# Kernel tuning notes

Hardware: AMD Instinct MI355X
Metric: run time of the kernel (lower is better)

## Reference

```python
import jax, jax.numpy as jnp
import numpy as np

N_USERS = 100_000
N_ITEMS = 200_000
N_EDGES = 1_000_000
D = 64        # in_size == every layer_size
L = 3         # number of NGCF layers
B = 4096      # BPR batch
SLOPE = 0.2   # LeakyReLU negative slope
EPS = 1e-12   # F.normalize eps


def setup_inputs() -> dict:
    key = jax.random.key(0)
    ks = jax.random.split(key, 11)
    s = 1.0 / np.sqrt(D)  # xavier-ish scale
    return dict(
        user_feat=jax.random.normal(ks[0], (N_USERS, D), jnp.float32) * s,
        item_feat=jax.random.normal(ks[1], (N_ITEMS, D), jnp.float32) * s,
        W1=jax.random.normal(ks[2], (L, D, D), jnp.float32) * s,
        b1=jnp.zeros((L, D), jnp.float32),
        W2=jax.random.normal(ks[3], (L, D, D), jnp.float32) * s,
        b2=jnp.zeros((L, D), jnp.float32),
        edge_src=jax.random.randint(ks[4], (N_EDGES,), 0, N_USERS),
        edge_dst=jax.random.randint(ks[5], (N_EDGES,), 0, N_ITEMS),
        users=jax.random.randint(ks[6], (B,), 0, N_USERS),
        pos_items=jax.random.randint(ks[7], (B,), 0, N_ITEMS),
        neg_items=jax.random.randint(ks[8], (B,), 0, N_ITEMS),
    )


def _act_norm(h):
    # LeakyReLU(0.2) -> (dropout=identity, eval) -> row-wise L2 normalize
    h = jax.nn.leaky_relu(h, SLOPE)
    n = jnp.linalg.norm(h, axis=1, keepdims=True)
    return h / jnp.maximum(n, EPS)


def _ngcf_forward(user_feat, item_feat, W1, b1, W2, b2, edge_src, edge_dst):
    ones = jnp.ones((edge_src.shape[0],), user_feat.dtype)
    deg_u = jax.ops.segment_sum(ones, edge_src, num_segments=N_USERS)  # out-degree of users
    deg_i = jax.ops.segment_sum(ones, edge_dst, num_segments=N_ITEMS)  # in-degree of items
    norm = (deg_u[edge_src] * deg_i[edge_dst]) ** -0.5  # [E], same for both directions
    norm = norm[:, None]

    hu, hi = user_feat, item_feat
    u_embeds, i_embeds = [hu], [hi]
    for l in range(L):
        # per-edge elementwise product term (shared between both directions)
        p = hu[edge_src] * hi[edge_dst]            # [E, D]
        pw = p @ W2[l] + b2[l]                     # [E, D]
        # user -> item messages, summed per item
        m_i = norm * ((hu @ W1[l] + b1[l])[edge_src] + pw)
        # item -> user messages, summed per user
        m_u = norm * ((hi @ W1[l] + b1[l])[edge_dst] + pw)
        hi_new = jax.ops.segment_sum(m_i, edge_dst, num_segments=N_ITEMS)
        hu_new = jax.ops.segment_sum(m_u, edge_src, num_segments=N_USERS)
        hu, hi = _act_norm(hu_new), _act_norm(hi_new)
        u_embeds.append(hu)
        i_embeds.append(hi)

    user_embd = jnp.concatenate(u_embeds, axis=1)  # [N_USERS, D*(L+1)]
    item_embd = jnp.concatenate(i_embeds, axis=1)  # [N_ITEMS, D*(L+1)]
    return user_embd, item_embd


def reference(user_feat, item_feat, W1, b1, W2, b2,
              edge_src, edge_dst, users, pos_items, neg_items):
    user_embd, item_embd = _ngcf_forward(
        user_feat, item_feat, W1, b1, W2, b2, edge_src, edge_dst)
    return (user_embd[users], item_embd[pos_items], item_embd[neg_items])
```

## Files before the change

### kernel.cpp

```cpp
#include <hip/hip_runtime.h>

#define NU 100000
#define NI 200000
#define NE 1000000
#define NB 4096
#define CAP 16384
#define NBS 98
#define NBD 98
#define NTI (NI / 16)
#define NTU (NU / 16)
#define DBKT 64
#define CAPD 65536
#define NBI 196
#define NBU 98

typedef __attribute__((ext_vector_type(8))) short bf16x8;
typedef __attribute__((ext_vector_type(4))) float f32x4;
typedef __attribute__((ext_vector_type(8))) unsigned short u16x8;

static __device__ __forceinline__ short f2bf(float f) {
  unsigned u = __builtin_bit_cast(unsigned, f);
  unsigned r = (u + 0x7fffu + ((u >> 16) & 1u)) >> 16;
  return (short)r;
}
static __device__ __forceinline__ float bf2f(unsigned short u) {
  return __builtin_bit_cast(float, ((unsigned)u) << 16);
}

__global__ __launch_bounds__(256) void binA_kernel(const int* __restrict__ src,
                                                   const int* __restrict__ dst,
                                                   int* __restrict__ gcur_s,
                                                   int* __restrict__ gcur_d,
                                                   int2* __restrict__ temp_s,
                                                   int2* __restrict__ temp_d) {
  __shared__ int lh[128], lbase[128], lpos[128];
  const int dir = blockIdx.x >> 9;
  const int cb = blockIdx.x & 511;
  const int lo = (int)(((long long)NE * cb) >> 9);
  const int hi = (int)(((long long)NE * (cb + 1)) >> 9);
  const int* key = dir ? dst : src;
  const int* oth = dir ? src : dst;
  int* gcur = dir ? gcur_d : gcur_s;
  int2* temp = dir ? temp_d : temp_s;
  const int shift = dir ? 11 : 10;
  const int tid = threadIdx.x;
  if (tid < 128) lh[tid] = 0;
  __syncthreads();
  for (int e = lo + tid; e < hi; e += 256) atomicAdd(&lh[key[e] >> shift], 1);
  __syncthreads();
  if (tid < 128) {
    const int c = lh[tid];
    lbase[tid] = c ? atomicAdd(&gcur[tid], c) : 0;
    lpos[tid] = 0;
  }
  __syncthreads();
  for (int e = lo + tid; e < hi; e += 256) {
    const int k = key[e];
    const int b = k >> shift;
    const int p = lbase[b] + atomicAdd(&lpos[b], 1);
    temp[(size_t)b * CAP + p] = make_int2(k, oth[e]);
  }
}

__global__ void bktscan_kernel(const int* __restrict__ gcur_s, const int* __restrict__ gcur_d,
                               int* __restrict__ bktofs_s, int* __restrict__ bktofs_d,
                               int* __restrict__ ofs_u, int* __restrict__ ofs_i) {
  const int t = threadIdx.x;
  if (t == 0) {
    int a = 0;
    for (int i = 0; i < NBS; ++i) { bktofs_s[i] = a; a += gcur_s[i]; }
    bktofs_s[NBS] = a;
    ofs_u[NU] = NE;
  }
  if (t == 1) {
    int a = 0;
    for (int i = 0; i < NBD; ++i) { bktofs_d[i] = a; a += gcur_d[i]; }
    bktofs_d[NBD] = a;
    ofs_i[NI] = NE;
  }
}

__global__ __launch_bounds__(256) void placeB_kernel(const int2* __restrict__ temp_s,
                                                     const int2* __restrict__ temp_d,
                                                     const int* __restrict__ gcur_s,
                                                     const int* __restrict__ gcur_d,
                                                     const int* __restrict__ bktofs_s,
                                                     const int* __restrict__ bktofs_d,
                                                     int* __restrict__ ofs_u, int* __restrict__ ofs_i,
                                                     int* __restrict__ by_src, int* __restrict__ by_dst) {
  __shared__ int cnt[2048];
  __shared__ int exc[2048];
  __shared__ int wsum[256];
  const bool isdst = blockIdx.x >= NBS;
  const int b = isdst ? (int)blockIdx.x - NBS : (int)blockIdx.x;
  const int shift = isdst ? 11 : 10;
  const int nodelo = b << shift;
  const int n = isdst ? NI : NU;
  const int2* temp = (isdst ? temp_d : temp_s) + (size_t)b * CAP;
  const int ecnt = (isdst ? gcur_d : gcur_s)[b];
  const int bbase = (isdst ? bktofs_d : bktofs_s)[b];
  int* ofs = isdst ? ofs_i : ofs_u;
  int* by = isdst ? by_dst : by_src;
  const int tid = threadIdx.x;
  const int NN = 1 << shift;

  for (int j = tid; j < NN; j += 256) cnt[j] = 0;
  __syncthreads();
  for (int k = tid; k < ecnt; k += 256) atomicAdd(&cnt[temp[k].x - nodelo], 1);
  __syncthreads();
  const int per = NN >> 8;
  int s = 0;
  for (int j = 0; j < per; ++j) s += cnt[tid * per + j];
  wsum[tid] = s;
  __syncthreads();
  for (int off = 1; off < 256; off <<= 1) {
    int t2 = (tid >= off) ? wsum[tid - off] : 0;
    __syncthreads();
    wsum[tid] += t2;
    __syncthreads();
  }
  int run = wsum[tid] - s;
  for (int j = 0; j < per; ++j) {
    const int idx = tid * per + j;
    exc[idx] = run;
    run += cnt[idx];
  }
  __syncthreads();
  for (int j = tid; j < NN; j += 256) {
    const int node = nodelo + j;
    if (node < n) ofs[node] = bbase + exc[j];
  }
  __syncthreads();
  for (int j = tid; j < NN; j += 256) cnt[j] = exc[j];
  __syncthreads();
  for (int k = tid; k < ecnt; k += 256) {
    const int2 t2 = temp[k];
    const int p = bbase + atomicAdd(&cnt[t2.x - nodelo], 1);
    by[p] = t2.y;
  }
}

__global__ __launch_bounds__(256) void dbinA_kernel(const int* __restrict__ ofs_i,
                                                    const int* __restrict__ ofs_u,
                                                    int* __restrict__ dgcur,
                                                    int* __restrict__ arena_i,
                                                    int* __restrict__ arena_u) {
  __shared__ int lh[DBKT], lbase[DBKT], lpos[DBKT];
  const bool item = blockIdx.x < NBI;
  const int b = item ? (int)blockIdx.x : (int)blockIdx.x - NBI;
  const int n = item ? NI : NU;
  const int* ofs = item ? ofs_i : ofs_u;
  int* cur = dgcur + (item ? 0 : DBKT);
  int* arena = item ? arena_i : arena_u;
  const int nodelo = b << 10;
  const int nodehi = min(nodelo + 1024, n);
  const int tid = threadIdx.x;
  if (tid < DBKT) lh[tid] = 0;
  __syncthreads();
  for (int node = nodelo + tid; node < nodehi; node += 256)
    atomicAdd(&lh[min(ofs[node + 1] - ofs[node], DBKT - 1)], 1);
  __syncthreads();
  if (tid < DBKT) {
    const int c = lh[tid];
    lbase[tid] = c ? atomicAdd(&cur[tid], c) : 0;
    lpos[tid] = 0;
  }
  __syncthreads();
  for (int node = nodelo + tid; node < nodehi; node += 256) {
    const int d = min(ofs[node + 1] - ofs[node], DBKT - 1);
    const int p = lbase[d] + atomicAdd(&lpos[d], 1);
    arena[d * CAPD + p] = node;
  }
}

__global__ void dbktscan_kernel(const int* __restrict__ dgcur,
                                int* __restrict__ dofs, int* __restrict__ dedge,
                                int* __restrict__ ofs2_i, int* __restrict__ ofs2_u) {
  const int t = threadIdx.x;
  if (t == 0) {
    int a = 0, e = 0;
    for (int d = 0; d < DBKT; ++d) { dofs[d] = a; dedge[d] = e; a += dgcur[d]; e += dgcur[d] * d; }
    dedge[DBKT] = NE;
    ofs2_i[NI] = NE;
  }
  if (t == 1) {
    int a = 0, e = 0;
    for (int d = 0; d < DBKT; ++d) {
      dofs[DBKT + d] = a; dedge[65 + d] = e;
      a += dgcur[DBKT + d]; e += dgcur[DBKT + d] * d;
    }
    dedge[65 + DBKT] = NE;
    ofs2_u[NU] = NE;
  }
}

__global__ __launch_bounds__(256) void dcompact_kernel(const int* __restrict__ dgcur,
                                                       const int* __restrict__ dofs,
                                                       const int* __restrict__ dedge,
                                                       const int* __restrict__ arena_i,
                                                       const int* __restrict__ arena_u,
                                                       int* __restrict__ perm_i, int* __restrict__ perm_u,
                                                       int* __restrict__ inv_i, int* __restrict__ inv_u,
                                                       int* __restrict__ ofs2_i, int* __restrict__ ofs2_u,
                                                       float* __restrict__ rs2_i, float* __restrict__ rs2_u) {
  const int bk = blockIdx.x;
  const bool item = bk < DBKT;
  const int d = item ? bk : bk - DBKT;
  const int cnt = dgcur[bk];
  const int nodebase = dofs[bk];
  const int edgebase = dedge[item ? d : 65 + d];
  const int* arena = item ? arena_i : arena_u;
  int* perm = item ? perm_i : perm_u;
  int* inv = item ? inv_i : inv_u;
  int* ofs2 = item ? ofs2_i : ofs2_u;
  float* rs2 = item ? rs2_i : rs2_u;
  const float rsv = d ? rsqrtf((float)d) : 0.f;
  for (int k = threadIdx.x; k < cnt; k += 256) {
    const int node = arena[d * CAPD + k];
    const int r = nodebase + k;
    perm[r] = node;
    inv[node] = r;
    ofs2[r] = edgebase + k * d;
    rs2[r] = rsv;
  }
}

__global__ __launch_bounds__(256) void remap3_kernel(const int* __restrict__ ofs_i,
                                                     const int* __restrict__ ofs_u,
                                                     const int* __restrict__ ofs2_i,
                                                     const int* __restrict__ ofs2_u,
                                                     const int* __restrict__ perm_i,
                                                     const int* __restrict__ perm_u,
                                                     const int* __restrict__ inv_i,
                                                     const int* __restrict__ inv_u,
                                                     const int* __restrict__ by_dst,
                                                     const int* __restrict__ by_src,
                                                     const float* __restrict__ rs2_u,
                                                     const float* __restrict__ rs2_i,
                                                     int* __restrict__ by2_dst,
                                                     int* __restrict__ by2_src,
                                                     float* __restrict__ c_i,
                                                     float* __restrict__ c_u) {
  int r = blockIdx.x * 256 + threadIdx.x;
  const int *ofs, *ofs2, *perm, *invo, *by;
  const float *rso, *rsw;
  int* by2;
  float* c;
  int rr;
  if (r < NI) {
    rr = r; ofs = ofs_i; ofs2 = ofs2_i; perm = perm_i; invo = inv_u;
    by = by_dst; rso = rs2_u; rsw = rs2_i; by2 = by2_dst; c = c_i;
  } else if (r < NI + NU) {
    rr = r - NI; ofs = ofs_u; ofs2 = ofs2_u; perm = perm_u; invo = inv_i;
    by = by_src; rso = rs2_i; rsw = rs2_u; by2 = by2_src; c = c_u;
  } else return;
  const int lo2 = ofs2[rr];
  const int d = ofs2[rr + 1] - lo2;
  float sum = 0.f;
  if (d > 0) {
    const int oo = ofs[perm[rr]];
    for (int k0 = 0; k0 < d; k0 += 4) {
      int v4[4], nv[4];
#pragma unroll
      for (int s = 0; s < 4; ++s) v4[s] = by[oo + min(k0 + s, d - 1)];
#pragma unroll
      for (int s = 0; s < 4; ++s) nv[s] = invo[v4[s]];
#pragma unroll
      for (int s = 0; s < 4; ++s)
        if (k0 + s < d) {
          by2[lo2 + k0 + s] = nv[s];
          sum += rso[nv[s]];
        }
    }
  }
  c[rr] = rsw[rr] * sum;
}

__global__ __launch_bounds__(256) void obuild_kernel(const int* __restrict__ users,
                                                     const int* __restrict__ pos,
                                                     const int* __restrict__ neg,
                                                     const int* __restrict__ inv_u,
                                                     const int* __restrict__ inv_i,
                                                     int* __restrict__ head_u,
                                                     int* __restrict__ head_i,
                                                     int* __restrict__ nxt) {
  const int s = blockIdx.x * 256 + threadIdx.x;
  if (s >= 3 * NB) return;
  const int which = s / NB, b = s - which * NB;
  const int row = (which == 0) ? users[b] : ((which == 1) ? pos[b] : neg[b]);
  int node;
  int* head;
  if (which == 0) { node = inv_u[row]; head = head_u; }
  else            { node = inv_i[row]; head = head_i; }
  nxt[s] = atomicExch(&head[node], s);
}

__global__ __launch_bounds__(256) void conv_kernel(const float* __restrict__ uf,
                                                   const float* __restrict__ itf,
                                                   const int* __restrict__ perm_u,
                                                   const int* __restrict__ perm_i,
                                                   const float* __restrict__ rs2_u,
                                                   const float* __restrict__ rs2_i,
                                                   unsigned short* __restrict__ hsu,
                                                   unsigned short* __restrict__ hsi) {
  int i = blockIdx.x * 256 + threadIdx.x;
  const int n4u = NU * 16;
  const float* in;
  const int* perm;
  const float* rs;
  unsigned short* outp;
  int j;
  if (i < n4u) {
    in = uf; perm = perm_u; rs = rs2_u; outp = hsu; j = i;
  } else if (i < n4u + NI * 16) {
    in = itf; perm = perm_i; rs = rs2_i; outp = hsi; j = i - n4u;
  } else return;
  const int rnew = j >> 4;
  const int grp = j & 15;
  const float rsn = rs[rnew];
  float4 v = *(const float4*)&in[(size_t)perm[rnew] * 64 + grp * 4];
  ushort4 o;
  o.x = (unsigned short)f2bf(v.x * rsn);
  o.y = (unsigned short)f2bf(v.y * rsn);
  o.z = (unsigned short)f2bf(v.z * rsn);
  o.w = (unsigned short)f2bf(v.w * rsn);
  *(ushort4*)&outp[(size_t)j * 4] = o;
}

__global__ __launch_bounds__(256) void layer_fused_kernel(const int* __restrict__ ofs2_i,
                                                          const int* __restrict__ ofs2_u,
                                                          const int* __restrict__ by2_dst,
                                                          const int* __restrict__ by2_src,
                                                          const float* __restrict__ rs2_u,
                                                          const float* __restrict__ rs2_i,
                                                          const float* __restrict__ c_i,
                                                          const float* __restrict__ c_u,
                                                          const unsigned short* __restrict__ hsu,
                                                          const unsigned short* __restrict__ hsi,
                                                          const float* __restrict__ W1,
                                                          const float* __restrict__ b1,
                                                          const float* __restrict__ W2,
                                                          const float* __restrict__ b2,
                                                          const int* __restrict__ head_i,
                                                          const int* __restrict__ head_u,
                                                          const int* __restrict__ nxt,
                                                          float* __restrict__ outp,
                                                          int stage,
                                                          unsigned short* __restrict__ hsi_new,
                                                          unsigned short* __restrict__ hsu_new) {
  __shared__ unsigned short wlds[8192];
  const int tid = threadIdx.x;
  const int lane = tid & 63;
  const int row16 = lane & 15;
  const int kg = lane >> 4;
  for (int ch = tid; ch < 1024; ch += 256) {
    const int w = ch >> 9;
    const int rem = ch & 511;
    const int nb = rem >> 7, kb = (rem >> 6) & 1, l2 = rem & 63;
    const int r16 = l2 & 15, kg2 = l2 >> 4;
    const float* W = w ? W2 : W1;
    unsigned short* dstp = &wlds[ch * 8];
#pragma unroll
    for (int j = 0; j < 8; ++j)
      dstp[j] = (unsigned short)f2bf(W[(kb * 32 + kg2 * 8 + j) * 64 + nb * 16 + r16]);
  }
  __syncthreads();

  float bsum[4];
#pragma unroll
  for (int nb = 0; nb < 4; ++nb) bsum[nb] = b1[nb * 16 + row16] + b2[nb * 16 + row16];

  const int wid = (blockIdx.x * 256 + tid) >> 6;
  const int nwaves = (gridDim.x * 256) >> 6;

  for (int t = wid; t < NTI + NTU; t += nwaves) {
    const bool item = t < NTI;
    const int tt = item ? t : t - NTI;
    const int* ofs = item ? ofs2_i : ofs2_u;
    const int* pay = item ? by2_dst : by2_src;
    const float* rsw = item ? rs2_i : rs2_u;
    const float* cc = item ? c_i : c_u;
    const int* head = item ? head_i : head_u;
    const unsigned short* hs = item ? hsu : hsi;
    const unsigned short* hsown = item ? hsi : hsu;
    unsigned short* hsnew = item ? hsi_new : hsu_new;
    const int r0 = tt * 16;
    const int node = r0 + row16;

    const int lo = ofs[node], hiE = ofs[node + 1];
    int rounds = (hiE - lo + 3) >> 2;
#pragma unroll
    for (int m = 1; m < 16; m <<= 1) rounds = max(rounds, __shfl_xor(rounds, m));

    float a0[8] = {0.f, 0.f, 0.f, 0.f, 0.f, 0.f, 0.f, 0.f};
    float a1[8] = {0.f, 0.f, 0.f, 0.f, 0.f, 0.f, 0.f, 0.f};
    for (int rd = 0; rd < rounds; ++rd) {
      const int i0 = lo + rd * 4;
      int nb4[4];
      float wt[4];
#pragma unroll
      for (int s = 0; s < 4; ++s) {
        const int idx = i0 + s;
        nb4[s] = pay[min(idx, NE - 1)];
        wt[s] = (idx < hiE) ? 1.f : 0.f;
      }
      u16x8 h0[4], h1[4];
#pragma unroll
      for (int s = 0; s < 4; ++s) {
        const unsigned short* hp = hs + (size_t)nb4[s] * 64 + kg * 8;
        h0[s] = *(const u16x8*)hp;
        h1[s] = *(const u16x8*)(hp + 32);
      }
#pragma unroll
      for (int s = 0; s < 4; ++s)
#pragma unroll
        for (int j = 0; j < 8; ++j) {
          a0[j] += wt[s] * bf2f(h0[s][j]);
          a1[j] += wt[s] * bf2f(h1[s][j]);
        }
    }

    const float rsn = rsw[node];
    const float cnode = cc[node];
    const unsigned short* hp = hsown + (size_t)node * 64 + kg * 8;
    const u16x8 hv0 = *(const u16x8*)hp;
    const u16x8 hv1 = *(const u16x8*)(hp + 32);
    bf16x8 ag[2], ap[2];
#pragma unroll
    for (int j = 0; j < 8; ++j) {
      ag[0][j] = f2bf(a0[j] * rsn);
      ag[1][j] = f2bf(a1[j] * rsn);
      ap[0][j] = f2bf(a0[j] * bf2f(hv0[j]));
      ap[1][j] = f2bf(a1[j] * bf2f(hv1[j]));
    }

    f32x4 acc[4];
#pragma unroll
    for (int nb = 0; nb < 4; ++nb) acc[nb] = (f32x4){0.f, 0.f, 0.f, 0.f};
    const unsigned short* wl = wlds + lane * 8;
#pragma unroll
    for (int nb = 0; nb < 4; ++nb)
#pragma unroll
      for (int kb = 0; kb < 2; ++kb) {
        const bf16x8 w1f = *(const bf16x8*)(wl + ((0 * 4 + nb) * 2 + kb) * 512);
        const bf16x8 w2f = *(const bf16x8*)(wl + ((1 * 4 + nb) * 2 + kb) * 512);
        acc[nb] = __builtin_amdgcn_mfma_f32_16x16x32_bf16(ag[kb], w1f, acc[nb], 0, 0, 0);
        acc[nb] = __builtin_amdgcn_mfma_f32_16x16x32_bf16(ap[kb], w2f, acc[nb], 0, 0, 0);
      }

    float cv[4], rsrow[4];
#pragma unroll
    for (int reg = 0; reg < 4; ++reg) {
      cv[reg] = __shfl(cnode, kg * 4 + reg);
      rsrow[reg] = __shfl(rsn, kg * 4 + reg);
    }
    float v[4][4];
    float ss[4] = {0.f, 0.f, 0.f, 0.f};
#pragma unroll
    for (int nb = 0; nb < 4; ++nb)
#pragma unroll
      for (int reg = 0; reg < 4; ++reg) {
        float x = acc[nb][reg] + cv[reg] * bsum[nb];
        x = (x > 0.f) ? x : 0.2f * x;
        v[nb][reg] = x;
        ss[reg] += x * x;
      }
#pragma unroll
    for (int m = 1; m < 16; m <<= 1)
#pragma unroll
      for (int reg = 0; reg < 4; ++reg) ss[reg] += __shfl_xor(ss[reg], m);
#pragma unroll
    for (int reg = 0; reg < 4; ++reg) {
      const int noder = r0 + kg * 4 + reg;
      const float invn = 1.0f / fmaxf(sqrtf(ss[reg]), 1e-12f);
      const float invs = invn * rsrow[reg];
      const size_t rowbase = (size_t)noder * 64;
#pragma unroll
      for (int nb = 0; nb < 4; ++nb)
        hsnew[rowbase + nb * 16 + row16] = (unsigned short)f2bf(v[nb][reg] * invs);
      int s = head[noder];
      while (s >= 0) {
        float* op = outp + (size_t)s * 256 + stage * 64;
#pragma unroll
        for (int nb = 0; nb < 4; ++nb) op[nb * 16 + row16] = v[nb][reg] * invn;
        s = nxt[s];
      }
    }
  }
}

__global__ __launch_bounds__(256) void gather_f32_kernel(const float* __restrict__ hu,
                                                         const float* __restrict__ hi,
                                                         const int* __restrict__ users,
                                                         const int* __restrict__ pos,
                                                         const int* __restrict__ neg,
                                                         float* __restrict__ out) {
  int t = blockIdx.x * 256 + threadIdx.x;
  if (t >= 3 * NB * 64) return;
  int j = t & 63;
  int b = (t >> 6) & (NB - 1);
  int which = t / (NB * 64);
  int row = (which == 0) ? users[b] : ((which == 1) ? pos[b] : neg[b]);
  const float* h = (which == 0) ? hu : hi;
  out[(size_t)which * NB * 256 + (size_t)b * 256 + j] = h[(size_t)row * 64 + j];
}

extern "C" void kernel_launch(void* const* d_in, const int* in_sizes, int n_in,
                              void* d_out, int out_size, void* d_ws, size_t ws_size,
                              hipStream_t stream) {
  (void)in_sizes; (void)n_in; (void)out_size; (void)ws_size;
  const float* user_feat = (const float*)d_in[0];
  const float* item_feat = (const float*)d_in[1];
  const float* W1 = (const float*)d_in[2];
  const float* b1 = (const float*)d_in[3];
  const float* W2 = (const float*)d_in[4];
  const float* b2 = (const float*)d_in[5];
  const int* edge_src = (const int*)d_in[6];
  const int* edge_dst = (const int*)d_in[7];
  const int* users = (const int*)d_in[8];
  const int* pos_items = (const int*)d_in[9];
  const int* neg_items = (const int*)d_in[10];
  float* out = (float*)d_out;

  char* base = (char*)d_ws;
  size_t ofsz = 0;
  auto alloc = [&](size_t bytes) -> char* {
    char* r = base + ofsz;
    ofsz += (bytes + 1023) & ~(size_t)1023;
    return r;
  };
  int* ofs_u = (int*)alloc((NU + 1) * 4);
  int* ofs_i = (int*)alloc((NI + 1) * 4);
  int* ofs2_u = (int*)alloc((NU + 1) * 4);
  int* ofs2_i = (int*)alloc((NI + 1) * 4);
  int* gcur_s = (int*)alloc(128 * 4);
  int* gcur_d = (int*)alloc(128 * 4);
  int* bktofs_s = (int*)alloc(128 * 4);
  int* bktofs_d = (int*)alloc(128 * 4);
  int* dgcur = (int*)alloc(2 * DBKT * 4);
  int* dofs = (int*)alloc(2 * DBKT * 4);
  int* dedge = (int*)alloc(2 * 65 * 4);
  int2* temp_s = (int2*)alloc((size_t)NBS * CAP * 8);
  int2* temp_d = (int2*)alloc((size_t)NBD * CAP * 8);
  int* by_src = (int*)alloc((size_t)NE * 4);
  int* by_dst = (int*)alloc((size_t)NE * 4);
  int* by2_src = (int*)alloc((size_t)NE * 4);
  int* by2_dst = (int*)alloc((size_t)NE * 4);
  int* arena_i = (int*)alloc((size_t)DBKT * CAPD * 4);
  int* arena_u = (int*)alloc((size_t)DBKT * CAPD * 4);
  int* perm_i = (int*)alloc((size_t)NI * 4);
  int* perm_u = (int*)alloc((size_t)NU * 4);
  int* inv_i = (int*)alloc((size_t)NI * 4);
  int* inv_u = (int*)alloc((size_t)NU * 4);
  float* rs2_u = (float*)alloc((size_t)NU * 4);
  float* rs2_i = (float*)alloc((size_t)NI * 4);
  float* c_u = (float*)alloc((size_t)NU * 4);
  float* c_i = (float*)alloc((size_t)NI * 4);
  int* head_u = (int*)alloc((size_t)NU * 4);
  int* head_i = (int*)alloc((size_t)NI * 4);
  int* onxt = (int*)alloc(3 * NB * 4);
  unsigned short* hsU0 = (unsigned short*)alloc((size_t)NU * 64 * 2);
  unsigned short* hsU1 = (unsigned short*)alloc((size_t)NU * 64 * 2);
  unsigned short* hsI0 = (unsigned short*)alloc((size_t)NI * 64 * 2);
  unsigned short* hsI1 = (unsigned short*)alloc((size_t)NI * 64 * 2);

  unsigned short* bufU[2] = {hsU1, hsU0};
  unsigned short* bufI[2] = {hsI1, hsI0};

  hipMemsetAsync(gcur_s, 0, 128 * 4, stream);
  hipMemsetAsync(gcur_d, 0, 128 * 4, stream);
  hipMemsetAsync(dgcur, 0, 2 * DBKT * 4, stream);
  hipMemsetAsync(head_u, 0xFF, (size_t)NU * 4, stream);
  hipMemsetAsync(head_i, 0xFF, (size_t)NI * 4, stream);
  binA_kernel<<<1024, 256, 0, stream>>>(edge_src, edge_dst, gcur_s, gcur_d, temp_s, temp_d);
  bktscan_kernel<<<1, 64, 0, stream>>>(gcur_s, gcur_d, bktofs_s, bktofs_d, ofs_u, ofs_i);
  placeB_kernel<<<NBS + NBD, 256, 0, stream>>>(temp_s, temp_d, gcur_s, gcur_d,
                                               bktofs_s, bktofs_d, ofs_u, ofs_i,
                                               by_src, by_dst);
  dbinA_kernel<<<NBI + NBU, 256, 0, stream>>>(ofs_i, ofs_u, dgcur, arena_i, arena_u);
  dbktscan_kernel<<<1, 64, 0, stream>>>(dgcur, dofs, dedge, ofs2_i, ofs2_u);
  dcompact_kernel<<<2 * DBKT, 256, 0, stream>>>(dgcur, dofs, dedge, arena_i, arena_u,
                                                perm_i, perm_u, inv_i, inv_u,
                                                ofs2_i, ofs2_u, rs2_i, rs2_u);
  remap3_kernel<<<(NI + NU + 255) / 256, 256, 0, stream>>>(ofs_i, ofs_u, ofs2_i, ofs2_u,
                                                           perm_i, perm_u, inv_i, inv_u,
                                                           by_dst, by_src, rs2_u, rs2_i,
                                                           by2_dst, by2_src, c_i, c_u);
  obuild_kernel<<<(3 * NB + 255) / 256, 256, 0, stream>>>(users, pos_items, neg_items,
                                                          inv_u, inv_i, head_u, head_i, onxt);
  conv_kernel<<<((NU + NI) * 16 + 255) / 256, 256, 0, stream>>>(
      user_feat, item_feat, perm_u, perm_i, rs2_u, rs2_i, hsU0, hsI0);

  gather_f32_kernel<<<(3 * NB * 64 + 255) / 256, 256, 0, stream>>>(
      user_feat, item_feat, users, pos_items, neg_items, out);

  const unsigned short* hsu = hsU0;
  const unsigned short* hsi = hsI0;
  for (int l = 0; l < 3; ++l) {
    unsigned short* hsu_new = bufU[l & 1];
    unsigned short* hsi_new = bufI[l & 1];
    layer_fused_kernel<<<2048, 256, 0, stream>>>(ofs2_i, ofs2_u, by2_dst, by2_src,
                                                 rs2_u, rs2_i, c_i, c_u,
                                                 hsu, hsi,
                                                 W1 + l * 4096, b1 + l * 64,
                                                 W2 + l * 4096, b2 + l * 64,
                                                 head_i, head_u, onxt, out, l + 1,
                                                 hsi_new, hsu_new);
    hsu = hsu_new;
    hsi = hsi_new;
  }
}
```

Baseline: 434.8 us.

## Fuse degree binning into placeB and split layer launch into item/user halves

Folds the degree-bucket histogram and arena placement into placeB_kernel, reusing the per-node counts already held in shared memory. This removes the separate dbinA kernel and its re-read of the offset arrays. The per-layer fused kernel is also split into two launches, one for item tiles and one for user tiles, each with its own tile range and grid size. The split could change load balance and adds a launch per layer.

```diff
diff --git a/kernel.cpp b/kernel.cpp
--- a/kernel.cpp
+++ b/kernel.cpp
@@ -11,8 +11,6 @@
 #define NTU (NU / 16)
 #define DBKT 64
 #define CAPD 65536
-#define NBI 196
-#define NBU 98
 
 typedef __attribute__((ext_vector_type(8))) short bf16x8;
 typedef __attribute__((ext_vector_type(4))) float f32x4;
@@ -87,10 +85,14 @@
                                                      const int* __restrict__ bktofs_s,
                                                      const int* __restrict__ bktofs_d,
                                                      int* __restrict__ ofs_u, int* __restrict__ ofs_i,
-                                                     int* __restrict__ by_src, int* __restrict__ by_dst) {
+                                                     int* __restrict__ by_src, int* __restrict__ by_dst,
+                                                     int* __restrict__ dgcur,
+                                                     int* __restrict__ arena_i,
+                                                     int* __restrict__ arena_u) {
   __shared__ int cnt[2048];
   __shared__ int exc[2048];
   __shared__ int wsum[256];
+  __shared__ int dlh[DBKT], dlb[DBKT], dlp[DBKT];
   const bool isdst = blockIdx.x >= NBS;
   const int b = isdst ? (int)blockIdx.x - NBS : (int)blockIdx.x;
   const int shift = isdst ? 11 : 10;
@@ -101,10 +103,13 @@
   const int bbase = (isdst ? bktofs_d : bktofs_s)[b];
   int* ofs = isdst ? ofs_i : ofs_u;
   int* by = isdst ? by_dst : by_src;
+  int* arena = isdst ? arena_i : arena_u;
+  int* dcur = dgcur + (isdst ? 0 : DBKT);
   const int tid = threadIdx.x;
   const int NN = 1 << shift;
 
   for (int j = tid; j < NN; j += 256) cnt[j] = 0;
+  if (tid < DBKT) dlh[tid] = 0;
   __syncthreads();
   for (int k = tid; k < ecnt; k += 256) atomicAdd(&cnt[temp[k].x - nodelo], 1);
   __syncthreads();
@@ -128,7 +133,25 @@
   __syncthreads();
   for (int j = tid; j < NN; j += 256) {
     const int node = nodelo + j;
-    if (node < n) ofs[node] = bbase + exc[j];
+    if (node < n) {
+      ofs[node] = bbase + exc[j];
+      atomicAdd(&dlh[min(cnt[j], DBKT - 1)], 1);
+    }
+  }
+  __syncthreads();
+  if (tid < DBKT) {
+    const int c = dlh[tid];
+    dlb[tid] = c ? atomicAdd(&dcur[tid], c) : 0;
+    dlp[tid] = 0;
+  }
+  __syncthreads();
+  for (int j = tid; j < NN; j += 256) {
+    const int node = nodelo + j;
+    if (node < n) {
+      const int d = min(cnt[j], DBKT - 1);
+      const int p = dlb[d] + atomicAdd(&dlp[d], 1);
+      arena[d * CAPD + p] = node;
+    }
   }
   __syncthreads();
   for (int j = tid; j < NN; j += 256) cnt[j] = exc[j];
@@ -137,39 +160,6 @@
     const int2 t2 = temp[k];
     const int p = bbase + atomicAdd(&cnt[t2.x - nodelo], 1);
     by[p] = t2.y;
-  }
-}
-
-__global__ __launch_bounds__(256) void dbinA_kernel(const int* __restrict__ ofs_i,
-                                                    const int* __restrict__ ofs_u,
-                                                    int* __restrict__ dgcur,
-                                                    int* __restrict__ arena_i,
-                                                    int* __restrict__ arena_u) {
-  __shared__ int lh[DBKT], lbase[DBKT], lpos[DBKT];
-  const bool item = blockIdx.x < NBI;
-  const int b = item ? (int)blockIdx.x : (int)blockIdx.x - NBI;
-  const int n = item ? NI : NU;
-  const int* ofs = item ? ofs_i : ofs_u;
-  int* cur = dgcur + (item ? 0 : DBKT);
-  int* arena = item ? arena_i : arena_u;
-  const int nodelo = b << 10;
-  const int nodehi = min(nodelo + 1024, n);
-  const int tid = threadIdx.x;
-  if (tid < DBKT) lh[tid] = 0;
-  __syncthreads();
-  for (int node = nodelo + tid; node < nodehi; node += 256)
-    atomicAdd(&lh[min(ofs[node + 1] - ofs[node], DBKT - 1)], 1);
-  __syncthreads();
-  if (tid < DBKT) {
-    const int c = lh[tid];
-    lbase[tid] = c ? atomicAdd(&cur[tid], c) : 0;
-    lpos[tid] = 0;
-  }
-  __syncthreads();
-  for (int node = nodelo + tid; node < nodehi; node += 256) {
-    const int d = min(ofs[node + 1] - ofs[node], DBKT - 1);
-    const int p = lbase[d] + atomicAdd(&lpos[d], 1);
-    arena[d * CAPD + p] = node;
   }
 }
 
@@ -345,7 +335,7 @@
                                                           const int* __restrict__ head_u,
                                                           const int* __restrict__ nxt,
                                                           float* __restrict__ outp,
-                                                          int stage,
+                                                          int stage, int t0, int t1,
                                                           unsigned short* __restrict__ hsi_new,
                                                           unsigned short* __restrict__ hsu_new) {
   __shared__ unsigned short wlds[8192];
@@ -373,7 +363,7 @@
   const int wid = (blockIdx.x * 256 + tid) >> 6;
   const int nwaves = (gridDim.x * 256) >> 6;
 
-  for (int t = wid; t < NTI + NTU; t += nwaves) {
+  for (int t = t0 + wid; t < t1; t += nwaves) {
     const bool item = t < NTI;
     const int tt = item ? t : t - NTI;
     const int* ofs = item ? ofs2_i : ofs2_u;
@@ -576,8 +566,7 @@
   bktscan_kernel<<<1, 64, 0, stream>>>(gcur_s, gcur_d, bktofs_s, bktofs_d, ofs_u, ofs_i);
   placeB_kernel<<<NBS + NBD, 256, 0, stream>>>(temp_s, temp_d, gcur_s, gcur_d,
                                                bktofs_s, bktofs_d, ofs_u, ofs_i,
-                                               by_src, by_dst);
-  dbinA_kernel<<<NBI + NBU, 256, 0, stream>>>(ofs_i, ofs_u, dgcur, arena_i, arena_u);
+                                               by_src, by_dst, dgcur, arena_i, arena_u);
   dbktscan_kernel<<<1, 64, 0, stream>>>(dgcur, dofs, dedge, ofs2_i, ofs2_u);
   dcompact_kernel<<<2 * DBKT, 256, 0, stream>>>(dgcur, dofs, dedge, arena_i, arena_u,
                                                 perm_i, perm_u, inv_i, inv_u,
@@ -599,13 +588,22 @@
   for (int l = 0; l < 3; ++l) {
     unsigned short* hsu_new = bufU[l & 1];
     unsigned short* hsi_new = bufI[l & 1];
-    layer_fused_kernel<<<2048, 256, 0, stream>>>(ofs2_i, ofs2_u, by2_dst, by2_src,
+    layer_fused_kernel<<<1376, 256, 0, stream>>>(ofs2_i, ofs2_u, by2_dst, by2_src,
                                                  rs2_u, rs2_i, c_i, c_u,
                                                  hsu, hsi,
                                                  W1 + l * 4096, b1 + l * 64,
                                                  W2 + l * 4096, b2 + l * 64,
                                                  head_i, head_u, onxt, out, l + 1,
+                                                 0, NTI,
                                                  hsi_new, hsu_new);
+    layer_fused_kernel<<<688, 256, 0, stream>>>(ofs2_i, ofs2_u, by2_dst, by2_src,
+                                                rs2_u, rs2_i, c_i, c_u,
+                                                hsu, hsi,
+                                                W1 + l * 4096, b1 + l * 64,
+                                                W2 + l * 4096, b2 + l * 64,
+                                                head_i, head_u, onxt, out, l + 1,
+                                                NTI, NTI + NTU,
+                                                hsi_new, hsu_new);
     hsu = hsu_new;
     hsi = hsi_new;
   }
```

Measured after the change: 463.2 us. 1.07x slower.
